# Performance work log

Hardware: AMD Instinct MI355X
Metric: run time of the kernel (lower is better)

## Reference

```python
import jax, jax.numpy as jnp
import numpy as np

N_STEPS = 8  # fixed-step RK4 over t in [0, 1]


def setup_inputs() -> dict:
    key = jax.random.key(0)
    ks = jax.random.split(key, 5)
    B, T, F, C = 64, 4096, 76, 15
    x = jax.random.normal(ks[0], (B, T, F), dtype=jnp.float32)
    # Conv1d(76->76, k=3) weights, PyTorch OIH layout, fan-in scaled
    conv_w = jax.random.normal(ks[1], (F, F, 3), dtype=jnp.float32) * (1.0 / np.sqrt(F * 3))
    conv_b = jax.random.normal(ks[2], (F,), dtype=jnp.float32) * 0.01
    final_w = jax.random.normal(ks[3], (C, F), dtype=jnp.float32) * (1.0 / np.sqrt(F))
    final_b = jax.random.normal(ks[4], (C,), dtype=jnp.float32) * 0.01
    return {"x": x, "conv_w": conv_w, "conv_b": conv_b,
            "final_w": final_w, "final_b": final_b}


def _func(h, conv_w, conv_b):
    # h: [B, F, T]; Conv1d k=3 pad=1 -> Tanh (the ODE vector field)
    y = jax.lax.conv_general_dilated(
        h, conv_w, window_strides=(1,), padding=[(1, 1)],
        dimension_numbers=("NCH", "OIH", "NCH"))
    return jnp.tanh(y + conv_b[None, :, None])


def reference(x, conv_w, conv_b, final_w, final_b):
    # x: [B, T, F] -> permute to channels-first for Conv1d
    h0 = jnp.transpose(x, (0, 2, 1))  # [B, F, T]
    dt = jnp.float32(1.0 / N_STEPS)

    def rk4_step(h, _):
        k1 = _func(h, conv_w, conv_b)
        k2 = _func(h + 0.5 * dt * k1, conv_w, conv_b)
        k3 = _func(h + 0.5 * dt * k2, conv_w, conv_b)
        k4 = _func(h + dt * k3, conv_w, conv_b)
        return h + (dt / 6.0) * (k1 + 2.0 * k2 + 2.0 * k3 + k4), None

    hT, _ = jax.lax.scan(rk4_step, h0, None, length=N_STEPS)
    # back to [B, T, F], then final Linear(F -> num_classes)
    out = jnp.einsum("bft,cf->btc", hT, final_w) + final_b
    return out
```

## Files before the change

kernel.cpp:

```cpp
#include <hip/hip_runtime.h>
#include <cstdint>
#include <cstddef>

#define F_CH 76
#define T_LEN 4096
#define B_TOT 64
#define C_CLS 15
#define NSTEP 8

#define W_OUT  112
#define HALO2  8
#define NBT    37
#define NKB    5
#define WSTR   88
#define SST    128
#define SROWS  130
#define TPB    768
#define HP     80

#define C2LOG2E 2.8853900817779268f

typedef __attribute__((ext_vector_type(8)))  __bf16 bf16x8;
typedef __attribute__((ext_vector_type(4)))  __bf16 bf16x4;
typedef __attribute__((ext_vector_type(16))) float  f32x16;

__device__ __forceinline__ int sw_off(int r, int v) {
    return r * SST + (((v) ^ (r & 15)) << 3);
}

__global__ __launch_bounds__(256) void pad_copy_kernel(
    const float* __restrict__ x, float* __restrict__ h, int b0)
{
    int bl = blockIdx.y;
    int q  = blockIdx.x * 256 + threadIdx.x;
    int t  = q / 20, c4 = (q - t * 20) * 4;
    float4 v = {0.f, 0.f, 0.f, 0.f};
    if (c4 < F_CH)
        v = *(const float4*)(x + ((size_t)(b0 + bl) * T_LEN + t) * F_CH + c4);
    *(float4*)(h + ((size_t)bl * T_LEN + t) * HP + c4) = v;
}

__global__ __launch_bounds__(256) void wprep_kernel(
    const float* __restrict__ cw, __bf16* __restrict__ wpb)
{
    int idx = blockIdx.x * 256 + threadIdx.x;
    if (idx >= 3 * 96 * WSTR) return;
    int tap = idx / (96 * WSTR);
    int rem = idx - tap * 96 * WSTR;
    int c = rem / WSTR, ci = rem - c * WSTR;
    float v = 0.0f;
    if (c < F_CH && ci < F_CH) v = cw[((size_t)c * F_CH + ci) * 3 + tap];
    wpb[idx] = (__bf16)v;
}

__global__ __launch_bounds__(TPB, 3) void rk4_step2_kernel(
    const float* __restrict__ hin, float* __restrict__ hout,
    const __bf16* __restrict__ wpb, const float* __restrict__ cb)
{
    __shared__ __bf16 s_lds[2][SROWS * SST];
    __shared__ float  cb_lds[96];

    const int b    = blockIdx.y;
    const int T0   = blockIdx.x * W_OUT;
    const int tid  = threadIdx.x;
    const int lane = tid & 63;
    const int l31  = lane & 31;
    const int l5   = lane >> 5;
    const int wv   = tid >> 6;
    const int ct   = wv >> 2;
    const int tq   = wv & 3;

    const int  rb  = tq * 32 + l31;
    const int  tg  = T0 - HALO2 + rb;
    const bool tok = (tg >= 0 && tg < T_LEN);

    if (tid < 256) {
        int bi = tid / 128, rr = (tid % 128) / 64, c = tid % 64;
        ((uint32_t*)&s_lds[bi][(rr ? (SROWS - 1) : 0) * SST])[c] = 0u;
    }
    if (tid < 96) cb_lds[tid] = (tid < F_CH) ? cb[tid] * C2LOG2E : 0.0f;

    float  hn[16];
    bf16x4 hpk[4];
    const float* hb = hin + (size_t)b * T_LEN * HP;
    #pragma unroll
    for (int q = 0; q < 4; ++q) {
        int c0 = ct * 32 + l5 * 4 + q * 8;
        float4 v = {0.f, 0.f, 0.f, 0.f};
        if (tok && c0 < HP) v = *(const float4*)(hb + (size_t)tg * HP + c0);
        hn[q*4+0]=v.x; hn[q*4+1]=v.y; hn[q*4+2]=v.z; hn[q*4+3]=v.w;
        hpk[q][0]=(__bf16)v.x; hpk[q][1]=(__bf16)v.y;
        hpk[q][2]=(__bf16)v.z; hpk[q][3]=(__bf16)v.w;
    }

    bf16x8 afr[3][NKB];
    #pragma unroll
    for (int tap = 0; tap < 3; ++tap)
        #pragma unroll
        for (int kb = 0; kb < NKB; ++kb)
            afr[tap][kb] = *(const bf16x8*)&wpb[((size_t)tap * 96 + ct * 32 + l31) * WSTR
                                                + kb * 16 + l5 * 8];

    const float dt = 0.125f;

    #pragma unroll 1
    for (int st = 0; st < 2; ++st) {
        #pragma unroll
        for (int q = 0; q < 4; ++q) {
            int c0 = ct * 32 + l5 * 4 + q * 8;
            if (c0 < HP)
                *(bf16x4*)&s_lds[0][sw_off(rb + 1, ct * 4 + q) + l5 * 4] = hpk[q];
        }
        __syncthreads();

        #pragma unroll 1
        for (int e = 0; e < 4; ++e) {
            const float we   = (e == 0 || e == 3) ? dt / 6.0f : dt / 3.0f;
            const float al   = (e == 2) ? dt : 0.5f * dt;
            const float al_t = tok ? al : 0.0f;

            const __bf16* sb = s_lds[e & 1];
            f32x16 a0 = {};
            #pragma unroll
            for (int tap = 0; tap < 3; ++tap) {
                #pragma unroll
                for (int kb = 0; kb < NKB; ++kb) {
                    bf16x8 bf = *(const bf16x8*)&sb[sw_off(rb + tap, kb * 2 + l5)];
                    a0 = __builtin_amdgcn_mfma_f32_32x32x16_bf16(afr[tap][kb], bf, a0, 0, 0, 0);
                }
            }

            __bf16* sw = s_lds[(e + 1) & 1];
            #pragma unroll
            for (int q = 0; q < 4; ++q) {
                int c0 = ct * 32 + l5 * 4 + q * 8;
                if (c0 >= HP) continue;
                bf16x4 p;
                #pragma unroll
                for (int j = 0; j < 4; ++j) {
                    float y  = fmaf(a0[q*4+j], C2LOG2E, cb_lds[c0 + j]);
                    float ex = __builtin_amdgcn_exp2f(y);
                    float kv = fmaf(-2.0f, __builtin_amdgcn_rcpf(ex + 1.0f), 1.0f);
                    hn[q*4+j] = fmaf(we, kv, hn[q*4+j]);
                    if (e < 3) p[j] = (__bf16)fmaf(al_t, kv, (float)hpk[q][j]);
                }
                if (e < 3)
                    *(bf16x4*)&sw[sw_off(rb + 1, ct * 4 + q) + l5 * 4] = p;
            }
            if (e < 3) __syncthreads();
        }

        if (st == 0) {
            #pragma unroll
            for (int i = 0; i < 16; ++i) hn[i] = tok ? hn[i] : 0.0f;
            #pragma unroll
            for (int q = 0; q < 4; ++q)
                #pragma unroll
                for (int j = 0; j < 4; ++j) hpk[q][j] = (__bf16)hn[q*4+j];
            __syncthreads();
        }
    }

    if (rb >= HALO2 && rb < HALO2 + W_OUT && tg < T_LEN) {
        float* ho = hout + ((size_t)b * T_LEN + tg) * HP;
        #pragma unroll
        for (int q = 0; q < 4; ++q) {
            int c0 = ct * 32 + l5 * 4 + q * 8;
            if (c0 < HP) {
                float4 v;
                v.x = hn[q*4+0]; v.y = hn[q*4+1];
                v.z = hn[q*4+2]; v.w = hn[q*4+3];
                *(float4*)(ho + c0) = v;
            }
        }
    }
}

__global__ __launch_bounds__(256) void final_kernel(
    const float* __restrict__ h, const float* __restrict__ fw,
    const float* __restrict__ fb, float* __restrict__ out, int b0)
{
    int bl = blockIdx.y;
    int t  = blockIdx.x * 256 + threadIdx.x;
    const float* hr = h + ((size_t)bl * T_LEN + t) * HP;
    float acc[C_CLS];
#pragma unroll
    for (int c = 0; c < C_CLS; ++c) acc[c] = fb[c];
#pragma unroll
    for (int qf = 0; qf < 19; ++qf) {
        float4 v = *(const float4*)(hr + qf * 4);
#pragma unroll
        for (int c = 0; c < C_CLS; ++c) {
            const float* w = fw + c * F_CH + qf * 4;
            acc[c] = fmaf(w[0], v.x, acc[c]);
            acc[c] = fmaf(w[1], v.y, acc[c]);
            acc[c] = fmaf(w[2], v.z, acc[c]);
            acc[c] = fmaf(w[3], v.w, acc[c]);
        }
    }
    float* ob = out + ((size_t)(b0 + bl) * T_LEN + t) * C_CLS;
#pragma unroll
    for (int c = 0; c < C_CLS; ++c) ob[c] = acc[c];
}

extern "C" void kernel_launch(void* const* d_in, const int* in_sizes, int n_in,
                              void* d_out, int out_size, void* d_ws, size_t ws_size,
                              hipStream_t stream)
{
    const float* x  = (const float*)d_in[0];
    const float* cw = (const float*)d_in[1];
    const float* cb = (const float*)d_in[2];
    const float* fw = (const float*)d_in[3];
    const float* fb = (const float*)d_in[4];
    float* out = (float*)d_out;

    const size_t FT = (size_t)T_LEN * HP;

    __bf16* WPB = (__bf16*)d_ws;
    const size_t wpbFloats = 12800;
    float* planes = (float*)d_ws + wpbFloats;

    size_t planeBytes = 2 * FT * sizeof(float);
    size_t avail = ws_size - wpbFloats * sizeof(float);
    int Bc = (int)(avail / planeBytes);
    if (Bc > B_TOT) Bc = B_TOT;
    if (Bc < 1) Bc = 1;

    float* H0 = planes;
    float* H1 = H0 + (size_t)Bc * FT;

    wprep_kernel<<<(3 * 96 * WSTR + 255) / 256, 256, 0, stream>>>(cw, WPB);

    for (int b0 = 0; b0 < B_TOT; b0 += Bc) {
        int bc = (B_TOT - b0 < Bc) ? (B_TOT - b0) : Bc;

        dim3 gP(T_LEN * 20 / 256, bc);
        pad_copy_kernel<<<gP, 256, 0, stream>>>(x, H0, b0);

        float* hcur = H0;
        float* hnxt = H1;
        dim3 gR(NBT, bc);
        for (int st2 = 0; st2 < NSTEP / 2; ++st2) {
            rk4_step2_kernel<<<gR, TPB, 0, stream>>>(hcur, hnxt, WPB, cb);
            float* tmp = hcur; hcur = hnxt; hnxt = tmp;
        }

        dim3 gF(T_LEN / 256, bc);
        final_kernel<<<gF, 256, 0, stream>>>(hcur, fw, fb, out, b0);
    }
}
```

Baseline: 816.0 us.

## Store intermediate ODE state in bf16 and widen time tiles to 144

The hidden-state planes between RK4 kernel launches now live in bf16 instead of fp32, which halves global traffic for the pad copy, the step kernels and the final linear layer. The tile width grows from 112 to 144 outputs with 15 waves per block. That lowers the share of halo recompute and the number of blocks. The bias is now read as a vector load. In exchange, the accumulated state is rounded to bf16 between every two RK4 steps, which loses precision, and the larger blocks use more LDS and registers, which may reduce occupancy.

New measurement: 891.0 us. +9.2%, slower.

```diff
diff --git a/kernel.cpp b/kernel.cpp
--- a/kernel.cpp
+++ b/kernel.cpp
@@ -8,14 +8,14 @@
 #define C_CLS 15
 #define NSTEP 8
 
-#define W_OUT  112
+#define W_OUT  144
 #define HALO2  8
-#define NBT    37
+#define NBT    29
 #define NKB    5
 #define WSTR   88
 #define SST    128
-#define SROWS  130
-#define TPB    768
+#define SROWS  162
+#define TPB    960
 #define HP     80
 
 #define C2LOG2E 2.8853900817779268f
@@ -23,13 +23,14 @@
 typedef __attribute__((ext_vector_type(8)))  __bf16 bf16x8;
 typedef __attribute__((ext_vector_type(4)))  __bf16 bf16x4;
 typedef __attribute__((ext_vector_type(16))) float  f32x16;
+typedef __attribute__((ext_vector_type(4)))  float  f32x4;
 
 __device__ __forceinline__ int sw_off(int r, int v) {
     return r * SST + (((v) ^ (r & 15)) << 3);
 }
 
 __global__ __launch_bounds__(256) void pad_copy_kernel(
-    const float* __restrict__ x, float* __restrict__ h, int b0)
+    const float* __restrict__ x, __bf16* __restrict__ h, int b0)
 {
     int bl = blockIdx.y;
     int q  = blockIdx.x * 256 + threadIdx.x;
@@ -37,7 +38,9 @@
     float4 v = {0.f, 0.f, 0.f, 0.f};
     if (c4 < F_CH)
         v = *(const float4*)(x + ((size_t)(b0 + bl) * T_LEN + t) * F_CH + c4);
-    *(float4*)(h + ((size_t)bl * T_LEN + t) * HP + c4) = v;
+    bf16x4 p;
+    p[0] = (__bf16)v.x; p[1] = (__bf16)v.y; p[2] = (__bf16)v.z; p[3] = (__bf16)v.w;
+    *(bf16x4*)(h + ((size_t)bl * T_LEN + t) * HP + c4) = p;
 }
 
 __global__ __launch_bounds__(256) void wprep_kernel(
@@ -53,8 +56,8 @@
     wpb[idx] = (__bf16)v;
 }
 
-__global__ __launch_bounds__(TPB, 3) void rk4_step2_kernel(
-    const float* __restrict__ hin, float* __restrict__ hout,
+__global__ __launch_bounds__(TPB, 4) void rk4_step2_kernel(
+    const __bf16* __restrict__ hin, __bf16* __restrict__ hout,
     const __bf16* __restrict__ wpb, const float* __restrict__ cb)
 {
     __shared__ __bf16 s_lds[2][SROWS * SST];
@@ -67,8 +70,8 @@
     const int l31  = lane & 31;
     const int l5   = lane >> 5;
     const int wv   = tid >> 6;
-    const int ct   = wv >> 2;
-    const int tq   = wv & 3;
+    const int ct   = wv / 5;
+    const int tq   = wv - ct * 5;
 
     const int  rb  = tq * 32 + l31;
     const int  tg  = T0 - HALO2 + rb;
@@ -82,15 +85,15 @@
 
     float  hn[16];
     bf16x4 hpk[4];
-    const float* hb = hin + (size_t)b * T_LEN * HP;
+    const __bf16* hb = hin + (size_t)b * T_LEN * HP;
     #pragma unroll
     for (int q = 0; q < 4; ++q) {
         int c0 = ct * 32 + l5 * 4 + q * 8;
-        float4 v = {0.f, 0.f, 0.f, 0.f};
-        if (tok && c0 < HP) v = *(const float4*)(hb + (size_t)tg * HP + c0);
-        hn[q*4+0]=v.x; hn[q*4+1]=v.y; hn[q*4+2]=v.z; hn[q*4+3]=v.w;
-        hpk[q][0]=(__bf16)v.x; hpk[q][1]=(__bf16)v.y;
-        hpk[q][2]=(__bf16)v.z; hpk[q][3]=(__bf16)v.w;
+        bf16x4 v = {};
+        if (tok && c0 < HP) v = *(const bf16x4*)(hb + (size_t)tg * HP + c0);
+        hpk[q] = v;
+        hn[q*4+0] = (float)v[0]; hn[q*4+1] = (float)v[1];
+        hn[q*4+2] = (float)v[2]; hn[q*4+3] = (float)v[3];
     }
 
     bf16x8 afr[3][NKB];
@@ -135,10 +138,11 @@
             for (int q = 0; q < 4; ++q) {
                 int c0 = ct * 32 + l5 * 4 + q * 8;
                 if (c0 >= HP) continue;
+                f32x4 bias = *(const f32x4*)&cb_lds[c0];
                 bf16x4 p;
                 #pragma unroll
                 for (int j = 0; j < 4; ++j) {
-                    float y  = fmaf(a0[q*4+j], C2LOG2E, cb_lds[c0 + j]);
+                    float y  = fmaf(a0[q*4+j], C2LOG2E, bias[j]);
                     float ex = __builtin_amdgcn_exp2f(y);
                     float kv = fmaf(-2.0f, __builtin_amdgcn_rcpf(ex + 1.0f), 1.0f);
                     hn[q*4+j] = fmaf(we, kv, hn[q*4+j]);
@@ -162,40 +166,41 @@
     }
 
     if (rb >= HALO2 && rb < HALO2 + W_OUT && tg < T_LEN) {
-        float* ho = hout + ((size_t)b * T_LEN + tg) * HP;
+        __bf16* ho = hout + ((size_t)b * T_LEN + tg) * HP;
         #pragma unroll
         for (int q = 0; q < 4; ++q) {
             int c0 = ct * 32 + l5 * 4 + q * 8;
             if (c0 < HP) {
-                float4 v;
-                v.x = hn[q*4+0]; v.y = hn[q*4+1];
-                v.z = hn[q*4+2]; v.w = hn[q*4+3];
-                *(float4*)(ho + c0) = v;
+                bf16x4 p;
+                p[0] = (__bf16)hn[q*4+0]; p[1] = (__bf16)hn[q*4+1];
+                p[2] = (__bf16)hn[q*4+2]; p[3] = (__bf16)hn[q*4+3];
+                *(bf16x4*)(ho + c0) = p;
             }
         }
     }
 }
 
 __global__ __launch_bounds__(256) void final_kernel(
-    const float* __restrict__ h, const float* __restrict__ fw,
+    const __bf16* __restrict__ h, const float* __restrict__ fw,
     const float* __restrict__ fb, float* __restrict__ out, int b0)
 {
     int bl = blockIdx.y;
     int t  = blockIdx.x * 256 + threadIdx.x;
-    const float* hr = h + ((size_t)bl * T_LEN + t) * HP;
+    const __bf16* hr = h + ((size_t)bl * T_LEN + t) * HP;
     float acc[C_CLS];
 #pragma unroll
     for (int c = 0; c < C_CLS; ++c) acc[c] = fb[c];
 #pragma unroll
     for (int qf = 0; qf < 19; ++qf) {
-        float4 v = *(const float4*)(hr + qf * 4);
+        bf16x4 v4 = *(const bf16x4*)(hr + qf * 4);
+        float v0 = (float)v4[0], v1 = (float)v4[1], v2 = (float)v4[2], v3 = (float)v4[3];
 #pragma unroll
         for (int c = 0; c < C_CLS; ++c) {
             const float* w = fw + c * F_CH + qf * 4;
-            acc[c] = fmaf(w[0], v.x, acc[c]);
-            acc[c] = fmaf(w[1], v.y, acc[c]);
-            acc[c] = fmaf(w[2], v.z, acc[c]);
-            acc[c] = fmaf(w[3], v.w, acc[c]);
+            acc[c] = fmaf(w[0], v0, acc[c]);
+            acc[c] = fmaf(w[1], v1, acc[c]);
+            acc[c] = fmaf(w[2], v2, acc[c]);
+            acc[c] = fmaf(w[3], v3, acc[c]);
         }
     }
     float* ob = out + ((size_t)(b0 + bl) * T_LEN + t) * C_CLS;
@@ -217,17 +222,17 @@
     const size_t FT = (size_t)T_LEN * HP;
 
     __bf16* WPB = (__bf16*)d_ws;
-    const size_t wpbFloats = 12800;
-    float* planes = (float*)d_ws + wpbFloats;
-
-    size_t planeBytes = 2 * FT * sizeof(float);
-    size_t avail = ws_size - wpbFloats * sizeof(float);
+    const size_t wpbBytes = 51200;
+    __bf16* planes = (__bf16*)((char*)d_ws + wpbBytes);
+
+    size_t planeBytes = 2 * FT * sizeof(__bf16);
+    size_t avail = ws_size - wpbBytes;
     int Bc = (int)(avail / planeBytes);
     if (Bc > B_TOT) Bc = B_TOT;
     if (Bc < 1) Bc = 1;
 
-    float* H0 = planes;
-    float* H1 = H0 + (size_t)Bc * FT;
+    __bf16* H0 = planes;
+    __bf16* H1 = H0 + (size_t)Bc * FT;
 
     wprep_kernel<<<(3 * 96 * WSTR + 255) / 256, 256, 0, stream>>>(cw, WPB);
 
@@ -237,12 +242,12 @@
         dim3 gP(T_LEN * 20 / 256, bc);
         pad_copy_kernel<<<gP, 256, 0, stream>>>(x, H0, b0);
 
-        float* hcur = H0;
-        float* hnxt = H1;
+        __bf16* hcur = H0;
+        __bf16* hnxt = H1;
         dim3 gR(NBT, bc);
         for (int st2 = 0; st2 < NSTEP / 2; ++st2) {
             rk4_step2_kernel<<<gR, TPB, 0, stream>>>(hcur, hnxt, WPB, cb);
-            float* tmp = hcur; hcur = hnxt; hnxt = tmp;
+            __bf16* tmp = hcur; hcur = hnxt; hnxt = tmp;
         }
 
         dim3 gF(T_LEN / 256, bc);
```
